# Performance work log

Measured on AMD Instinct MI355X. Metric: run time of the kernel, lower is better.

## Reference

```python
import jax, jax.numpy as jnp
import numpy as np

EMB = 1024; H = 8; HD = EMB // H // 2  # head_dim = 64, q/k use 2*H heads of HD; v uses H heads of 2*HD
FF = 4096; DEPTH = 1
LAM_INIT = float(0.8 - 0.6 * np.exp(-0.3 * DEPTH))

def setup_inputs() -> dict:
    key = jax.random.key(0)
    ks = jax.random.split(key, 12)
    s = lambda k, sh, sc: jax.random.normal(k, sh, jnp.float32) * sc
    return {
        'x': s(ks[0], (2, 2048, EMB), 1.0),
        'ln1_w': jnp.ones((EMB,), jnp.float32), 'ln1_b': jnp.zeros((EMB,), jnp.float32),
        'Wq': s(ks[1], (EMB, EMB), 0.02), 'Wk': s(ks[2], (EMB, EMB), 0.02),
        'Wv': s(ks[3], (EMB, EMB), 0.02), 'Wo': s(ks[4], (EMB, EMB), 0.02),
        'lq1': s(ks[5], (HD,), 0.1), 'lk1': s(ks[6], (HD,), 0.1),
        'lq2': s(ks[7], (HD,), 0.1), 'lk2': s(ks[8], (HD,), 0.1),
        'subln_w': jnp.ones((2 * HD,), jnp.float32),
        'ln2_w': jnp.ones((EMB,), jnp.float32), 'ln2_b': jnp.zeros((EMB,), jnp.float32),
        'W1': s(ks[9], (EMB, FF), 0.02), 'b1': jnp.zeros((FF,), jnp.float32),
        'W2': s(ks[10], (FF, EMB), 0.02), 'b2': jnp.zeros((EMB,), jnp.float32),
    }

def _ln(x, w, b):
    m = jnp.mean(x, -1, keepdims=True)
    v = jnp.var(x, -1, keepdims=True)
    return (x - m) * jax.lax.rsqrt(v + 1e-5) * w + b

def _rms(x, w):
    return x * jax.lax.rsqrt(jnp.mean(x * x, -1, keepdims=True) + 1e-5) * w

def reference(x, ln1_w, ln1_b, Wq, Wk, Wv, Wo, lq1, lk1, lq2, lk2, subln_w, ln2_w, ln2_b, W1, b1, W2, b2):
    B, N, _ = x.shape
    h = _ln(x, ln1_w, ln1_b)
    q = (h @ Wq).reshape(B, N, 2 * H, HD) * (HD ** -0.5)
    k = (h @ Wk).reshape(B, N, 2 * H, HD)
    v = (h @ Wv).reshape(B, N, H, 2 * HD)
    # dual softmax attention maps: [B, 2H, N, N]
    attn = jax.nn.softmax(jnp.einsum('bihd,bjhd->bhij', q, k), axis=-1)
    attn = attn.reshape(B, H, 2, N, N)
    lam = jnp.exp(jnp.sum(lq1 * lk1)) - jnp.exp(jnp.sum(lq2 * lk2)) + LAM_INIT
    a = attn[:, :, 0] - lam * attn[:, :, 1]  # differential attention [B,H,N,N]
    o = jnp.einsum('bhij,bjhd->bihd', a, v)  # [B,N,H,2*HD]
    o = _rms(o, subln_w) * (1.0 - LAM_INIT)
    x = x + o.reshape(B, N, EMB) @ Wo
    h = _ln(x, ln2_w, ln2_b)
    return x + (jax.nn.gelu(h @ W1 + b1, approximate=False) @ W2 + b2)
```

## Files before the change

kernel.cpp:

```cpp
#include <hip/hip_runtime.h>


typedef unsigned short u16;
typedef unsigned int u32;
typedef __attribute__((ext_vector_type(8))) __bf16 bf16x8;
typedef __attribute__((ext_vector_type(4))) float f32x4;
typedef __attribute__((ext_vector_type(4))) u32 u32x4;
typedef __attribute__((ext_vector_type(2))) u32 u32x2;

#define LOG2E 1.4426950408889634f
#define LAM_INIT 0.355509068f
#define ONE_MINUS_LAM_INIT 0.644490932f

__device__ __forceinline__ float bf2f(u16 x) {
  u32 u = ((u32)x) << 16;
  return __builtin_bit_cast(float, u);
}
__device__ __forceinline__ u16 f2bf(float f) {
  u32 u = __builtin_bit_cast(u32, f);
  u32 r = (u + 0x7FFFu + ((u >> 16) & 1u)) >> 16;
  return (u16)r;
}
__device__ __forceinline__ u32 cvtpk(float lo, float hi) {
  u32 r;
  asm("v_cvt_pk_bf16_f32 %0, %1, %2" : "=v"(r) : "v"(lo), "v"(hi));
  return r;
}
__device__ __forceinline__ float ldf(const void* p, size_t i, bool f32) {
  return f32 ? ((const float*)p)[i] : bf2f(((const u16*)p)[i]);
}
__device__ __forceinline__ void async16(const u16* g, u16* l) {
  __builtin_amdgcn_global_load_lds((const __attribute__((address_space(1))) u32*)g,
                                   (__attribute__((address_space(3))) u32*)l, 16, 0, 0);
}
__device__ __forceinline__ bf16x8 ld8(const u16* p) { return *(const bf16x8*)p; }

__global__ void detect_kernel(const u32* x, int* flag) {
  int e = (x[threadIdx.x] >> 7) & 0xFF;
  unsigned long long m = __ballot(e >= 90 && e <= 150);
  if (threadIdx.x == 0) flag[0] = (__popcll(m) >= 40) ? 1 : 0;
}

__global__ void lam_kernel(const void* lq1, const void* lk1, const void* lq2,
                           const void* lk2, const int* flag, float* out) {
  const bool f32 = flag[0] == 0;
  int L = threadIdx.x;
  float a = ldf(lq1, L, f32) * ldf(lk1, L, f32);
  float c = ldf(lq2, L, f32) * ldf(lk2, L, f32);
#pragma unroll
  for (int m = 1; m < 64; m <<= 1) { a += __shfl_xor(a, m); c += __shfl_xor(c, m); }
  if (L == 0) out[0] = __expf(a) - __expf(c) + LAM_INIT;
}

__device__ __forceinline__ void unpack8(u32x4 u, float* f) {
#pragma unroll
  for (int i = 0; i < 4; ++i) {
    f[2 * i] = bf2f((u16)(u[i] & 0xffffu));
    f[2 * i + 1] = bf2f((u16)(u[i] >> 16));
  }
}

template <bool XRAW>
__global__ __launch_bounds__(256) void ln_kernel(const void* __restrict__ x,
                                                 const void* __restrict__ w,
                                                 const void* __restrict__ b,
                                                 const int* __restrict__ flag,
                                                 u16* __restrict__ out) {
  const bool f32 = flag[0] == 0;
  const int row = blockIdx.x * 4 + (threadIdx.x >> 6);
  const int L = threadIdx.x & 63;
  float xv[16];
  if (XRAW && f32) {
    const f32x4* xr = (const f32x4*)((const float*)x + (size_t)row * 1024 + L * 16);
#pragma unroll
    for (int i = 0; i < 4; ++i) {
      f32x4 vv = xr[i];
#pragma unroll
      for (int j = 0; j < 4; ++j) xv[i * 4 + j] = vv[j];
    }
  } else {
    const u16* xr = (const u16*)x + (size_t)row * 1024 + L * 16;
    unpack8(*(const u32x4*)xr, xv);
    unpack8(*(const u32x4*)(xr + 8), xv + 8);
  }
  float s = 0.f, sq = 0.f;
#pragma unroll
  for (int i = 0; i < 16; ++i) { s += xv[i]; sq += xv[i] * xv[i]; }
#pragma unroll
  for (int m = 1; m < 64; m <<= 1) { s += __shfl_xor(s, m); sq += __shfl_xor(sq, m); }
  float mean = s * (1.0f / 1024.0f);
  float var = sq * (1.0f / 1024.0f) - mean * mean;
  float rstd = rsqrtf(var + 1e-5f);
  u32 pk[8];
#pragma unroll
  for (int i = 0; i < 8; ++i) {
    float w0 = ldf(w, L * 16 + 2 * i, f32), w1 = ldf(w, L * 16 + 2 * i + 1, f32);
    float b0 = ldf(b, L * 16 + 2 * i, f32), b1v = ldf(b, L * 16 + 2 * i + 1, f32);
    float v0 = (xv[2 * i] - mean) * rstd * w0 + b0;
    float v1 = (xv[2 * i + 1] - mean) * rstd * w1 + b1v;
    pk[i] = (u32)f2bf(v0) | ((u32)f2bf(v1) << 16);
  }
  u32x4 o0 = {pk[0], pk[1], pk[2], pk[3]};
  u32x4 o1 = {pk[4], pk[5], pk[6], pk[7]};
  *(u32x4*)(out + (size_t)row * 1024 + L * 16) = o0;
  *(u32x4*)(out + (size_t)row * 1024 + L * 16 + 8) = o1;
}

__global__ __launch_bounds__(256) void twc_kernel(const void* __restrict__ s0,
                                                  const void* __restrict__ s1,
                                                  const void* __restrict__ s2,
                                                  u16* __restrict__ dst, int sstride,
                                                  int dstride, size_t soff, size_t dzoff,
                                                  const int* __restrict__ flag) {
  __shared__ __align__(16) u16 tile[64][72];
  const bool f32 = flag[0] == 0;
  const void* src = blockIdx.z == 0 ? s0 : (blockIdx.z == 1 ? s1 : s2);
  u16* dz = dst + (size_t)blockIdx.z * dzoff;
  const int r0 = blockIdx.y * 64, c0 = blockIdx.x * 64;
  const int t = threadIdx.x;
  const int rr = t >> 3, cc = t & 7;
#pragma unroll
  for (int i = 0; i < 2; ++i) {
    int row = rr + i * 32;
    size_t idx = (size_t)(r0 + row) * sstride + c0 + cc * 8 + soff;
    if (f32) {
      const f32x4* s = (const f32x4*)((const float*)src + idx);
      f32x4 a = s[0], b = s[1];
      union { u16 t16[8]; u32x4 v; } u_;
#pragma unroll
      for (int j = 0; j < 4; ++j) { u_.t16[j] = f2bf(a[j]); u_.t16[4 + j] = f2bf(b[j]); }
      *(u32x4*)(&tile[row][cc * 8]) = u_.v;
    } else {
      *(u32x4*)(&tile[row][cc * 8]) = *(const u32x4*)((const u16*)src + idx);
    }
  }
  __syncthreads();
  u16* d = dz + (size_t)c0 * dstride + r0;
#pragma unroll
  for (int i = 0; i < 2; ++i) {
    int n = rr + i * 32;
    union { u16 t16[8]; u32x4 v; } u_;
#pragma unroll
    for (int j = 0; j < 8; ++j) u_.t16[j] = tile[cc * 8 + j][n];
    *(u32x4*)(d + (size_t)n * dstride + cc * 8) = u_.v;
  }
}

enum { EP_NONE = 0, EP_RES = 2, EP_GELU = 3, EP_BIASRES = 4, EP_QKV = 5 };

template <int TM, int EPI, bool RESRAW, bool OUTFLEX>
__global__ __launch_bounds__(256, 2) void gemm_bt(
    const u16* __restrict__ A, const u16* __restrict__ Bt, void* __restrict__ Cv,
    int M, int N, int K, const void* __restrict__ bias, int boff,
    const void* __restrict__ res, const int* __restrict__ flag,
    u16* __restrict__ kout, u16* __restrict__ vtout) {
  constexpr int MT = TM / 32;
  __shared__ __align__(16) u16 lds[TM * 64 + 128 * 64];
  const int t = threadIdx.x;
  const int w = t >> 6, L = t & 63;
  const int quad = L >> 4, l16 = L & 15;
  const int m0 = blockIdx.y * TM, n0 = blockIdx.x * 128;
  const int wm = (TM == 128) ? (w >> 1) * 64 : (w & 1) * 32;
  const int wn = (TM == 128) ? (w & 1) * 64 : (w >> 1) * 64;
  const int srow = L >> 3, spc = L & 7;
  const int sc = spc ^ srow;
  constexpr int BBASE = TM * 64;

  f32x4 acc[MT][4] = {};
  const u16* Ab = A + (size_t)m0 * K;
  const u16* Bb = Bt + (size_t)n0 * K;

  for (int kt = 0; kt < K; kt += 64) {
#pragma unroll
    for (int r = 0; r < TM / 32; ++r) {
      int row = r * 32 + w * 8 + srow;
      async16(Ab + (size_t)row * K + kt + sc * 8, &lds[row * 64 + spc * 8]);
    }
#pragma unroll
    for (int r = 0; r < 4; ++r) {
      int row = r * 32 + w * 8 + srow;
      async16(Bb + (size_t)row * K + kt + sc * 8, &lds[BBASE + row * 64 + spc * 8]);
    }
    __syncthreads();
#pragma unroll
    for (int ks = 0; ks < 2; ++ks) {
      bf16x8 af[MT], bfr[4];
#pragma unroll
      for (int mt = 0; mt < MT; ++mt) {
        int row = wm + mt * 16 + l16;
        af[mt] = ld8(&lds[row * 64 + (((ks * 4 + quad) ^ (l16 & 7)) * 8)]);
      }
#pragma unroll
      for (int nt = 0; nt < 4; ++nt) {
        int row = wn + nt * 16 + l16;
        bfr[nt] = ld8(&lds[BBASE + row * 64 + (((ks * 4 + quad) ^ (l16 & 7)) * 8)]);
      }
#pragma unroll
      for (int mt = 0; mt < MT; ++mt)
#pragma unroll
        for (int nt = 0; nt < 4; ++nt)
          acc[mt][nt] =
              __builtin_amdgcn_mfma_f32_16x16x32_bf16(af[mt], bfr[nt], acc[mt][nt], 0, 0, 0);
    }
    __syncthreads();
  }

  const bool f32 = flag[0] == 0;
#pragma unroll
  for (int mt = 0; mt < MT; ++mt) {
#pragma unroll
    for (int nt = 0; nt < 4; ++nt) {
      int col = n0 + wn + nt * 16 + l16;
      float bv = 0.f;
      if (EPI == EP_GELU || EPI == EP_BIASRES) bv = ldf(bias, (size_t)boff + col, f32);
#pragma unroll
      for (int r = 0; r < 4; ++r) {
        int row = m0 + wm + mt * 16 + quad * 4 + r;
        float v = acc[mt][nt][r];
        if (EPI == EP_GELU) {
          v += bv;
          v = 0.5f * v * (1.0f + erff(v * 0.70710678118654752f));
        }
        if (EPI == EP_RES || EPI == EP_BIASRES) {
          size_t ri = (size_t)row * N + col;
          float rv = RESRAW ? ldf(res, ri, f32) : bf2f(((const u16*)res)[ri]);
          v += rv;
          if (EPI == EP_BIASRES) v += bv;
        }
        if (EPI == EP_QKV) {
          if (col < 1024) {
            ((u16*)Cv)[(size_t)row * 1024 + col] = f2bf(v * 0.125f);
          } else if (col < 2048) {
            kout[(size_t)row * 1024 + (col - 1024)] = f2bf(v);
          } else {
            int c2 = col - 2048;
            int bb = row >> 11, n = row & 2047, hh = c2 >> 7, d = c2 & 127;
            vtout[(size_t)((bb * 8 + hh) * 128 + d) * 2048 + n] = f2bf(v);
          }
        } else {
          size_t ci = (size_t)row * N + col;
          if (OUTFLEX && f32)
            ((float*)Cv)[ci] = v;
          else
            ((u16*)Cv)[ci] = f2bf(v);
        }
      }
    }
  }
}

__global__ __launch_bounds__(256, 2) void attn_kernel(
    const u16* __restrict__ q, const u16* __restrict__ k, const u16* __restrict__ vT,
    const float* __restrict__ lamp, const void* __restrict__ subw,
    const int* __restrict__ flag, u16* __restrict__ o) {
  __shared__ __align__(16) u16 lds[24576];
  const int t = threadIdx.x, w = t >> 6, L = t & 63;
  const int quad = L >> 4, l16 = L & 15;
  const int bid = ((blockIdx.x & 7) << 6) | (blockIdx.x >> 3);
  const int qt = bid & 31, h = (bid >> 5) & 7, b = bid >> 8;
  const int q0 = qt * 64;
  const int comp = w >> 1, rh = (w & 1) * 32;
  const int srow = L >> 3, spc = L & 7, sc = spc ^ srow;
  const u16* vb = vT + (size_t)(b * 8 + h) * (128 * 2048);
  const int pbase = 16384 + w * 2048;

  auto stageK = [&](int kt) {
#pragma unroll
    for (int r = 0; r < 4; ++r) {
      int row = r * 32 + w * 8 + srow;
      int c_ = row >> 6, key = row & 63;
      async16(k + ((size_t)(b * 2048 + kt + key) * 1024 + (2 * h + c_) * 64 + sc * 8),
              &lds[row * 64 + spc * 8]);
    }
  };
  auto stageV = [&](int kt) {
#pragma unroll
    for (int r = 0; r < 4; ++r) {
      int dim = r * 32 + w * 8 + srow;
      async16(vb + (size_t)dim * 2048 + kt + sc * 8, &lds[8192 + dim * 64 + spc * 8]);
    }
  };

  stageK(0);
  stageV(0);
#pragma unroll
  for (int r = 0; r < 4; ++r) {
    int row = r * 32 + w * 8 + srow;
    int c_ = row >> 6, qr = row & 63;
    async16(q + ((size_t)(b * 2048 + q0 + qr) * 1024 + (2 * h + c_) * 64 + sc * 8),
            &lds[16384 + row * 64 + spc * 8]);
  }
  __syncthreads();
  bf16x8 qf[2][2];
#pragma unroll
  for (int mt = 0; mt < 2; ++mt)
#pragma unroll
    for (int ks = 0; ks < 2; ++ks) {
      int row = rh + mt * 16 + l16;
      qf[mt][ks] =
          ld8(&lds[16384 + comp * 4096 + row * 64 + (((ks * 4 + quad) ^ (l16 & 7)) * 8)]);
    }

  float mst[2] = {-1.0e30f, -1.0e30f};
  float mstl[2] = {-1.0e30f, -1.0e30f};
  float lst[2] = {0.f, 0.f};
  f32x4 oacc[8][2] = {};

  for (int ti = 0; ti < 32; ++ti) {
    f32x4 s[4][2] = {};
#pragma unroll
    for (int ks = 0; ks < 2; ++ks) {
      bf16x8 kf[4];
#pragma unroll
      for (int nt = 0; nt < 4; ++nt) {
        int row = nt * 16 + l16;
        kf[nt] = ld8(&lds[comp * 4096 + row * 64 + (((ks * 4 + quad) ^ (l16 & 7)) * 8)]);
      }
#pragma unroll
      for (int nt = 0; nt < 4; ++nt)
#pragma unroll
        for (int mt = 0; mt < 2; ++mt)
          s[nt][mt] = __builtin_amdgcn_mfma_f32_16x16x32_bf16(kf[nt], qf[mt][ks], s[nt][mt], 0, 0, 0);
    }

#pragma unroll
    for (int mt = 0; mt < 2; ++mt) {
      float mx = -3.0e38f;
#pragma unroll
      for (int nt = 0; nt < 4; ++nt)
#pragma unroll
        for (int r = 0; r < 4; ++r) mx = fmaxf(mx, s[nt][mt][r]);
      mx = fmaxf(mx, __shfl_xor(mx, 16));
      mx = fmaxf(mx, __shfl_xor(mx, 32));
      if (__ballot(mx > mst[mt] + 8.0f)) {
        float mnew = fmaxf(mst[mt], mx);
        float al = exp2f((mst[mt] - mnew) * LOG2E);
        mst[mt] = mnew;
        mstl[mt] = mnew * LOG2E;
        lst[mt] *= al;
#pragma unroll
        for (int nt = 0; nt < 8; ++nt)
#pragma unroll
          for (int r = 0; r < 4; ++r) oacc[nt][mt][r] *= al;
      }
      float ps = 0.f;
#pragma unroll
      for (int nt = 0; nt < 4; ++nt)
#pragma unroll
        for (int r = 0; r < 4; ++r) {
          float p = exp2f(__builtin_fmaf(s[nt][mt][r], LOG2E, -mstl[mt]));
          s[nt][mt][r] = p;
          ps += p;
        }
      ps += __shfl_xor(ps, 16);
      ps += __shfl_xor(ps, 32);
      lst[mt] += ps;
    }

#pragma unroll
    for (int mt = 0; mt < 2; ++mt) {
      int prow = mt * 16 + l16;
#pragma unroll
      for (int nt = 0; nt < 4; ++nt) {
        int pc = (nt * 2 + (quad >> 1)) ^ (l16 & 7);
        u32x2 pk2 = {cvtpk(s[nt][mt][0], s[nt][mt][1]), cvtpk(s[nt][mt][2], s[nt][mt][3])};
        *(u32x2*)(&lds[pbase + prow * 64 + pc * 8 + (quad & 1) * 4]) = pk2;
      }
    }
    __syncthreads();
    if (ti + 1 < 32) stageK((ti + 1) * 64);

#pragma unroll
    for (int ks = 0; ks < 2; ++ks) {
      bf16x8 pf[2];
#pragma unroll
      for (int mt = 0; mt < 2; ++mt) {
        int row = mt * 16 + l16;
        pf[mt] = ld8(&lds[pbase + row * 64 + (((ks * 4 + quad) ^ (l16 & 7)) * 8)]);
      }
#pragma unroll
      for (int nt = 0; nt < 8; ++nt) {
        int dim = nt * 16 + l16;
        bf16x8 vf = ld8(&lds[8192 + dim * 64 + (((ks * 4 + quad) ^ (l16 & 7)) * 8)]);
#pragma unroll
        for (int mt = 0; mt < 2; ++mt)
          oacc[nt][mt] = __builtin_amdgcn_mfma_f32_16x16x32_bf16(vf, pf[mt], oacc[nt][mt], 0, 0, 0);
      }
    }
    __syncthreads();
    if (ti + 1 < 32) stageV((ti + 1) * 64);
  }

#pragma unroll
  for (int mt = 0; mt < 2; ++mt) {
    float inv = 1.0f / lst[mt];
#pragma unroll
    for (int nt = 0; nt < 8; ++nt)
#pragma unroll
      for (int r = 0; r < 4; ++r) oacc[nt][mt][r] *= inv;
  }

  float* cb = (float*)lds;
  if (comp == 1) {
#pragma unroll
    for (int mt = 0; mt < 2; ++mt) {
      int rowc = rh + mt * 16 + l16;
#pragma unroll
      for (int nt = 0; nt < 8; ++nt)
        *(f32x4*)(&cb[rowc * 132 + nt * 16 + quad * 4]) = oacc[nt][mt];
    }
  }
  __syncthreads();
  if (comp == 0) {
    const bool f32 = flag[0] == 0;
    float lam = lamp[0];
    float sw[8][4];
#pragma unroll
    for (int nt = 0; nt < 8; ++nt)
#pragma unroll
      for (int r = 0; r < 4; ++r) sw[nt][r] = ldf(subw, nt * 16 + quad * 4 + r, f32);
#pragma unroll
    for (int mt = 0; mt < 2; ++mt) {
      int rowc = rh + mt * 16 + l16;
      float dv[8][4];
      float sq = 0.f;
#pragma unroll
      for (int nt = 0; nt < 8; ++nt) {
        f32x4 c2 = *(const f32x4*)(&cb[rowc * 132 + nt * 16 + quad * 4]);
#pragma unroll
        for (int r = 0; r < 4; ++r) {
          float d = oacc[nt][mt][r] - lam * c2[r];
          dv[nt][r] = d;
          sq += d * d;
        }
      }
      sq += __shfl_xor(sq, 16);
      sq += __shfl_xor(sq, 32);
      float rms = rsqrtf(sq * (1.0f / 128.0f) + 1e-5f);
      size_t rowg = (size_t)(b * 2048 + q0 + rowc) * 1024 + h * 128;
#pragma unroll
      for (int nt = 0; nt < 8; ++nt) {
        float v0 = dv[nt][0] * rms * sw[nt][0] * ONE_MINUS_LAM_INIT;
        float v1 = dv[nt][1] * rms * sw[nt][1] * ONE_MINUS_LAM_INIT;
        float v2 = dv[nt][2] * rms * sw[nt][2] * ONE_MINUS_LAM_INIT;
        float v3 = dv[nt][3] * rms * sw[nt][3] * ONE_MINUS_LAM_INIT;
        u32x2 pk2 = {cvtpk(v0, v1), cvtpk(v2, v3)};
        *(u32x2*)(o + rowg + nt * 16 + quad * 4) = pk2;
      }
    }
  }
}

extern "C" void kernel_launch(void* const* d_in, const int* in_sizes, int n_in,
                              void* d_out, int out_size, void* d_ws, size_t ws_size,
                              hipStream_t stream) {
  (void)in_sizes; (void)n_in; (void)out_size; (void)ws_size;
  const void* x = d_in[0];
  const void* ln1w = d_in[1];
  const void* ln1b = d_in[2];
  const void* Wq = d_in[3];
  const void* Wk = d_in[4];
  const void* Wv = d_in[5];
  const void* Wo = d_in[6];
  const void* lq1 = d_in[7];
  const void* lk1 = d_in[8];
  const void* lq2 = d_in[9];
  const void* lk2 = d_in[10];
  const void* subw = d_in[11];
  const void* ln2w = d_in[12];
  const void* ln2b = d_in[13];
  const void* W1 = d_in[14];
  const void* b1 = d_in[15];
  const void* W2 = d_in[16];
  const void* b2 = d_in[17];

  char* ws = (char*)d_ws;
  const size_t MB = 1u << 20;
  u16* A = (u16*)ws;
  u16* B = (u16*)(ws + 8 * MB);
  u16* C = (u16*)(ws + 16 * MB);
  u16* D = (u16*)(ws + 24 * MB);
  u16* E = (u16*)(ws + 32 * MB);
  float* lam = (float*)(ws + 40 * MB);
  int* flag = (int*)(ws + 40 * MB + 64);
  u16* W2Th = D + 2097152;

  detect_kernel<<<dim3(1), dim3(64), 0, stream>>>((const u32*)x, flag);
  lam_kernel<<<dim3(1), dim3(64), 0, stream>>>(lq1, lk1, lq2, lk2, flag, lam);
  ln_kernel<true><<<dim3(1024), dim3(256), 0, stream>>>(x, ln1w, ln1b, flag, A);

  twc_kernel<<<dim3(16, 16, 3), dim3(256), 0, stream>>>(Wq, Wk, Wv, E, 1024, 1024, 0,
                                                        1048576, flag);
  gemm_bt<64, EP_QKV, false, false><<<dim3(24, 64), dim3(256), 0, stream>>>(
      A, E, B, 4096, 3072, 1024, nullptr, 0, nullptr, flag, C, D);

  attn_kernel<<<dim3(512), dim3(256), 0, stream>>>(B, C, D, lam, subw, flag, A);

  twc_kernel<<<dim3(16, 16, 1), dim3(256), 0, stream>>>(Wo, Wo, Wo, D, 1024, 1024, 0, 0,
                                                        flag);
  gemm_bt<64, EP_RES, true, false><<<dim3(8, 64), dim3(256), 0, stream>>>(
      A, D, E, 4096, 1024, 1024, nullptr, 0, x, flag, nullptr, nullptr);
  ln_kernel<false><<<dim3(1024), dim3(256), 0, stream>>>(E, ln2w, ln2b, flag, A);

  for (int hh = 0; hh < 2; ++hh) {
    twc_kernel<<<dim3(32, 16, 1), dim3(256), 0, stream>>>(W1, W1, W1, D, 4096, 1024,
                                                          (size_t)hh * 2048, 0, flag);
    twc_kernel<<<dim3(16, 32, 1), dim3(256), 0, stream>>>(
        W2, W2, W2, W2Th, 1024, 2048, (size_t)hh * 2048 * 1024, 0, flag);
    gemm_bt<128, EP_GELU, false, false><<<dim3(16, 32), dim3(256), 0, stream>>>(
        A, D, B, 4096, 2048, 1024, b1, hh * 2048, nullptr, flag, nullptr, nullptr);
    if (hh == 0) {
      gemm_bt<64, EP_BIASRES, false, true><<<dim3(8, 64), dim3(256), 0, stream>>>(
          B, W2Th, d_out, 4096, 1024, 2048, b2, 0, E, flag, nullptr, nullptr);
    } else {
      gemm_bt<64, EP_RES, true, true><<<dim3(8, 64), dim3(256), 0, stream>>>(
          B, W2Th, d_out, 4096, 1024, 2048, nullptr, 0, d_out, flag, nullptr, nullptr);
    }
  }
}
```

Baseline: 478.7 us.

## Double-buffer LDS tiles in GEMM and attention to overlap loads with MFMA

Adds a double-buffered K-loop to the GEMM (enabled for the Wo, W1 and W2 GEMMs but not QKV) and double-buffers K/V tiles in the attention kernel. The next tile is prefetched into the alternate buffer while MFMAs run on the current one, and the number of barriers per iteration drops. Static shared memory becomes dynamic, so attention now needs 80KB and the 128-row GEMM 64KB of LDS. That may cut occupancy below the 2 blocks per CU the launch bounds target.

```diff
diff --git a/kernel.cpp b/kernel.cpp
--- a/kernel.cpp
+++ b/kernel.cpp
@@ -148,14 +148,15 @@
 
 enum { EP_NONE = 0, EP_RES = 2, EP_GELU = 3, EP_BIASRES = 4, EP_QKV = 5 };
 
-template <int TM, int EPI, bool RESRAW, bool OUTFLEX>
+template <int TM, int EPI, bool RESRAW, bool OUTFLEX, bool DB>
 __global__ __launch_bounds__(256, 2) void gemm_bt(
     const u16* __restrict__ A, const u16* __restrict__ Bt, void* __restrict__ Cv,
     int M, int N, int K, const void* __restrict__ bias, int boff,
     const void* __restrict__ res, const int* __restrict__ flag,
     u16* __restrict__ kout, u16* __restrict__ vtout) {
   constexpr int MT = TM / 32;
-  __shared__ __align__(16) u16 lds[TM * 64 + 128 * 64];
+  constexpr int HALF = TM * 64 + 128 * 64;
+  extern __shared__ __align__(16) u16 lds[];
   const int t = threadIdx.x;
   const int w = t >> 6, L = t & 63;
   const int quad = L >> 4, l16 = L & 15;
@@ -164,36 +165,37 @@
   const int wn = (TM == 128) ? (w & 1) * 64 : (w >> 1) * 64;
   const int srow = L >> 3, spc = L & 7;
   const int sc = spc ^ srow;
-  constexpr int BBASE = TM * 64;
 
   f32x4 acc[MT][4] = {};
   const u16* Ab = A + (size_t)m0 * K;
   const u16* Bb = Bt + (size_t)n0 * K;
 
-  for (int kt = 0; kt < K; kt += 64) {
+  auto stage = [&](int kt, int bsel) {
+    u16* base = lds + bsel * HALF;
 #pragma unroll
     for (int r = 0; r < TM / 32; ++r) {
       int row = r * 32 + w * 8 + srow;
-      async16(Ab + (size_t)row * K + kt + sc * 8, &lds[row * 64 + spc * 8]);
+      async16(Ab + (size_t)row * K + kt + sc * 8, &base[row * 64 + spc * 8]);
     }
 #pragma unroll
     for (int r = 0; r < 4; ++r) {
       int row = r * 32 + w * 8 + srow;
-      async16(Bb + (size_t)row * K + kt + sc * 8, &lds[BBASE + row * 64 + spc * 8]);
-    }
-    __syncthreads();
+      async16(Bb + (size_t)row * K + kt + sc * 8, &base[TM * 64 + row * 64 + spc * 8]);
+    }
+  };
+  auto ktile = [&](const u16* base) {
 #pragma unroll
     for (int ks = 0; ks < 2; ++ks) {
       bf16x8 af[MT], bfr[4];
 #pragma unroll
       for (int mt = 0; mt < MT; ++mt) {
         int row = wm + mt * 16 + l16;
-        af[mt] = ld8(&lds[row * 64 + (((ks * 4 + quad) ^ (l16 & 7)) * 8)]);
+        af[mt] = ld8(&base[row * 64 + (((ks * 4 + quad) ^ (l16 & 7)) * 8)]);
       }
 #pragma unroll
       for (int nt = 0; nt < 4; ++nt) {
         int row = wn + nt * 16 + l16;
-        bfr[nt] = ld8(&lds[BBASE + row * 64 + (((ks * 4 + quad) ^ (l16 & 7)) * 8)]);
+        bfr[nt] = ld8(&base[TM * 64 + row * 64 + (((ks * 4 + quad) ^ (l16 & 7)) * 8)]);
       }
 #pragma unroll
       for (int mt = 0; mt < MT; ++mt)
@@ -202,7 +204,23 @@
           acc[mt][nt] =
               __builtin_amdgcn_mfma_f32_16x16x32_bf16(af[mt], bfr[nt], acc[mt][nt], 0, 0, 0);
     }
-    __syncthreads();
+  };
+
+  if (DB) {
+    const int nst = K >> 6;
+    stage(0, 0);
+    for (int st = 0; st < nst; ++st) {
+      __syncthreads();
+      if (st + 1 < nst) stage((st + 1) << 6, (st + 1) & 1);
+      ktile(lds + (st & 1) * HALF);
+    }
+  } else {
+    for (int kt = 0; kt < K; kt += 64) {
+      stage(kt, 0);
+      __syncthreads();
+      ktile(lds);
+      __syncthreads();
+    }
   }
 
   const bool f32 = flag[0] == 0;
@@ -253,7 +271,8 @@
     const u16* __restrict__ q, const u16* __restrict__ k, const u16* __restrict__ vT,
     const float* __restrict__ lamp, const void* __restrict__ subw,
     const int* __restrict__ flag, u16* __restrict__ o) {
-  __shared__ __align__(16) u16 lds[24576];
+  extern __shared__ __align__(16) u16 lds[];
+  constexpr int VB = 16384, PB = 32768;
   const int t = threadIdx.x, w = t >> 6, L = t & 63;
   const int quad = L >> 4, l16 = L & 15;
   const int bid = ((blockIdx.x & 7) << 6) | (blockIdx.x >> 3);
@@ -262,33 +281,34 @@
   const int comp = w >> 1, rh = (w & 1) * 32;
   const int srow = L >> 3, spc = L & 7, sc = spc ^ srow;
   const u16* vb = vT + (size_t)(b * 8 + h) * (128 * 2048);
-  const int pbase = 16384 + w * 2048;
-
-  auto stageK = [&](int kt) {
+  const int pbase = PB + w * 2048;
+
+  auto stageK = [&](int kt, int bsel) {
 #pragma unroll
     for (int r = 0; r < 4; ++r) {
       int row = r * 32 + w * 8 + srow;
       int c_ = row >> 6, key = row & 63;
       async16(k + ((size_t)(b * 2048 + kt + key) * 1024 + (2 * h + c_) * 64 + sc * 8),
-              &lds[row * 64 + spc * 8]);
+              &lds[bsel * 8192 + row * 64 + spc * 8]);
     }
   };
-  auto stageV = [&](int kt) {
+  auto stageV = [&](int kt, int bsel) {
 #pragma unroll
     for (int r = 0; r < 4; ++r) {
       int dim = r * 32 + w * 8 + srow;
-      async16(vb + (size_t)dim * 2048 + kt + sc * 8, &lds[8192 + dim * 64 + spc * 8]);
+      async16(vb + (size_t)dim * 2048 + kt + sc * 8,
+              &lds[VB + bsel * 8192 + dim * 64 + spc * 8]);
     }
   };
 
-  stageK(0);
-  stageV(0);
+  stageK(0, 0);
+  stageV(0, 0);
 #pragma unroll
   for (int r = 0; r < 4; ++r) {
     int row = r * 32 + w * 8 + srow;
     int c_ = row >> 6, qr = row & 63;
     async16(q + ((size_t)(b * 2048 + q0 + qr) * 1024 + (2 * h + c_) * 64 + sc * 8),
-            &lds[16384 + row * 64 + spc * 8]);
+            &lds[PB + row * 64 + spc * 8]);
   }
   __syncthreads();
   bf16x8 qf[2][2];
@@ -298,7 +318,7 @@
     for (int ks = 0; ks < 2; ++ks) {
       int row = rh + mt * 16 + l16;
       qf[mt][ks] =
-          ld8(&lds[16384 + comp * 4096 + row * 64 + (((ks * 4 + quad) ^ (l16 & 7)) * 8)]);
+          ld8(&lds[PB + comp * 4096 + row * 64 + (((ks * 4 + quad) ^ (l16 & 7)) * 8)]);
     }
 
   float mst[2] = {-1.0e30f, -1.0e30f};
@@ -307,6 +327,13 @@
   f32x4 oacc[8][2] = {};
 
   for (int ti = 0; ti < 32; ++ti) {
+    __syncthreads();
+    const int bb = ti & 1;
+    if (ti + 1 < 32) {
+      stageK((ti + 1) * 64, bb ^ 1);
+      stageV((ti + 1) * 64, bb ^ 1);
+    }
+
     f32x4 s[4][2] = {};
 #pragma unroll
     for (int ks = 0; ks < 2; ++ks) {
@@ -314,7 +341,8 @@
 #pragma unroll
       for (int nt = 0; nt < 4; ++nt) {
         int row = nt * 16 + l16;
-        kf[nt] = ld8(&lds[comp * 4096 + row * 64 + (((ks * 4 + quad) ^ (l16 & 7)) * 8)]);
+        kf[nt] = ld8(&lds[bb * 8192 + comp * 4096 + row * 64 +
+                          (((ks * 4 + quad) ^ (l16 & 7)) * 8)]);
       }
 #pragma unroll
       for (int nt = 0; nt < 4; ++nt)
@@ -367,8 +395,6 @@
         *(u32x2*)(&lds[pbase + prow * 64 + pc * 8 + (quad & 1) * 4]) = pk2;
       }
     }
-    __syncthreads();
-    if (ti + 1 < 32) stageK((ti + 1) * 64);
 
 #pragma unroll
     for (int ks = 0; ks < 2; ++ks) {
@@ -381,14 +407,13 @@
 #pragma unroll
       for (int nt = 0; nt < 8; ++nt) {
         int dim = nt * 16 + l16;
-        bf16x8 vf = ld8(&lds[8192 + dim * 64 + (((ks * 4 + quad) ^ (l16 & 7)) * 8)]);
+        bf16x8 vf = ld8(&lds[VB + bb * 8192 + dim * 64 +
+                             (((ks * 4 + quad) ^ (l16 & 7)) * 8)]);
 #pragma unroll
         for (int mt = 0; mt < 2; ++mt)
           oacc[nt][mt] = __builtin_amdgcn_mfma_f32_16x16x32_bf16(vf, pf[mt], oacc[nt][mt], 0, 0, 0);
       }
     }
-    __syncthreads();
-    if (ti + 1 < 32) stageV((ti + 1) * 64);
   }
 
 #pragma unroll
@@ -400,6 +425,7 @@
       for (int r = 0; r < 4; ++r) oacc[nt][mt][r] *= inv;
   }
 
+  __syncthreads();
   float* cb = (float*)lds;
   if (comp == 1) {
 #pragma unroll
@@ -485,20 +511,24 @@
   int* flag = (int*)(ws + 40 * MB + 64);
   u16* W2Th = D + 2097152;
 
+  const int g64_1 = (64 * 64 + 128 * 64) * 2;
+  const int g64_2 = g64_1 * 2;
+  const int g128_2 = (128 * 64 + 128 * 64) * 2 * 2;
+
   detect_kernel<<<dim3(1), dim3(64), 0, stream>>>((const u32*)x, flag);
   lam_kernel<<<dim3(1), dim3(64), 0, stream>>>(lq1, lk1, lq2, lk2, flag, lam);
   ln_kernel<true><<<dim3(1024), dim3(256), 0, stream>>>(x, ln1w, ln1b, flag, A);
 
   twc_kernel<<<dim3(16, 16, 3), dim3(256), 0, stream>>>(Wq, Wk, Wv, E, 1024, 1024, 0,
                                                         1048576, flag);
-  gemm_bt<64, EP_QKV, false, false><<<dim3(24, 64), dim3(256), 0, stream>>>(
+  gemm_bt<64, EP_QKV, false, false, false><<<dim3(24, 64), dim3(256), g64_1, stream>>>(
       A, E, B, 4096, 3072, 1024, nullptr, 0, nullptr, flag, C, D);
 
-  attn_kernel<<<dim3(512), dim3(256), 0, stream>>>(B, C, D, lam, subw, flag, A);
+  attn_kernel<<<dim3(512), dim3(256), 81920, stream>>>(B, C, D, lam, subw, flag, A);
 
   twc_kernel<<<dim3(16, 16, 1), dim3(256), 0, stream>>>(Wo, Wo, Wo, D, 1024, 1024, 0, 0,
                                                         flag);
-  gemm_bt<64, EP_RES, true, false><<<dim3(8, 64), dim3(256), 0, stream>>>(
+  gemm_bt<64, EP_RES, true, false, true><<<dim3(8, 64), dim3(256), g64_2, stream>>>(
       A, D, E, 4096, 1024, 1024, nullptr, 0, x, flag, nullptr, nullptr);
   ln_kernel<false><<<dim3(1024), dim3(256), 0, stream>>>(E, ln2w, ln2b, flag, A);
 
@@ -507,13 +537,13 @@
                                                           (size_t)hh * 2048, 0, flag);
     twc_kernel<<<dim3(16, 32, 1), dim3(256), 0, stream>>>(
         W2, W2, W2, W2Th, 1024, 2048, (size_t)hh * 2048 * 1024, 0, flag);
-    gemm_bt<128, EP_GELU, false, false><<<dim3(16, 32), dim3(256), 0, stream>>>(
+    gemm_bt<128, EP_GELU, false, false, true><<<dim3(16, 32), dim3(256), g128_2, stream>>>(
         A, D, B, 4096, 2048, 1024, b1, hh * 2048, nullptr, flag, nullptr, nullptr);
     if (hh == 0) {
-      gemm_bt<64, EP_BIASRES, false, true><<<dim3(8, 64), dim3(256), 0, stream>>>(
+      gemm_bt<64, EP_BIASRES, false, true, true><<<dim3(8, 64), dim3(256), g64_2, stream>>>(
           B, W2Th, d_out, 4096, 1024, 2048, b2, 0, E, flag, nullptr, nullptr);
     } else {
-      gemm_bt<64, EP_RES, true, true><<<dim3(8, 64), dim3(256), 0, stream>>>(
+      gemm_bt<64, EP_RES, true, true, true><<<dim3(8, 64), dim3(256), g64_2, stream>>>(
           B, W2Th, d_out, 4096, 1024, 2048, nullptr, 0, d_out, flag, nullptr, nullptr);
     }
   }
```

Measured after the change: 464.8 us. 1.03x faster.
